# Optimization experiments

Measured on AMD Instinct MI355X. Metric: run time of the kernel, lower is better.

Reference implementation:

```python
import jax, jax.numpy as jnp
import numpy as np

WS = 7           # window side
N = WS * WS      # tokens per window = 49
DIM = 384
H = 12
HD = DIM // H    # 32
BW = 2048        # num_windows * batch
NW = 4           # windows per image (mask batch)
SCALE = 1.0 / float(np.sqrt(HD))


def _rel_index():
    coords = np.stack(np.meshgrid(np.arange(WS), np.arange(WS), indexing='ij'))  # (2,7,7)
    flat = coords.reshape(2, -1)                      # (2,49)
    rel = flat[:, :, None] - flat[:, None, :]         # (2,49,49)
    rel = rel.transpose(1, 2, 0).copy()               # (49,49,2)
    rel[..., 0] += WS - 1
    rel[..., 1] += WS - 1
    rel[..., 0] *= 2 * WS - 1
    return jnp.asarray(rel.sum(-1), dtype=jnp.int32)  # (49,49)


def setup_inputs() -> dict:
    key = jax.random.key(0)
    ks = jax.random.split(key, 16)
    f32 = jnp.float32
    se = jax.random.normal(ks[0], (BW, N, DIM), dtype=f32)
    de = jax.random.normal(ks[1], (BW, N, DIM), dtype=f32)
    mask = jnp.where(jax.random.uniform(ks[2], (NW, N, N)) < 0.1, f32(-1e9), f32(0.0))
    s = 0.02
    w_v_se = jax.random.normal(ks[3], (DIM, DIM), dtype=f32) * s
    b_v_se = jnp.zeros((DIM,), dtype=f32)
    w_qkv = jax.random.normal(ks[4], (3 * DIM, DIM), dtype=f32) * s
    b_qkv = jnp.zeros((3 * DIM,), dtype=f32)
    w_proj_se = jax.random.normal(ks[5], (DIM, DIM), dtype=f32) * s
    b_proj_se = jnp.zeros((DIM,), dtype=f32)
    w_proj_de = jax.random.normal(ks[6], (DIM, DIM), dtype=f32) * s
    b_proj_de = jnp.zeros((DIM,), dtype=f32)
    rpb = jax.random.normal(ks[7], ((2 * WS - 1) ** 2, H), dtype=f32) * s  # (169,12)
    rel_idx = _rel_index()
    return {
        'se': se, 'de': de, 'mask': mask,
        'w_v_se': w_v_se, 'b_v_se': b_v_se,
        'w_qkv': w_qkv, 'b_qkv': b_qkv,
        'w_proj_se': w_proj_se, 'b_proj_se': b_proj_se,
        'w_proj_de': w_proj_de, 'b_proj_de': b_proj_de,
        'rpb': rpb, 'rel_idx': rel_idx,
    }


def reference(se, de, mask, w_v_se, b_v_se, w_qkv, b_qkv,
              w_proj_se, b_proj_se, w_proj_de, b_proj_de, rpb, rel_idx):
    B_, N_, C = se.shape
    # qkv from de (coa=False branch)
    qkv = (de @ w_qkv.T + b_qkv).reshape(B_, N_, 3, H, HD).transpose(2, 0, 3, 1, 4)
    q, k, v_de = qkv[0], qkv[1], qkv[2]                 # (B_,H,N,HD)
    v_se = (se @ w_v_se.T + b_v_se).reshape(B_, N_, H, HD).transpose(0, 2, 1, 3)
    attn = jnp.einsum('bhnd,bhmd->bhnm', q * SCALE, k)  # (B_,H,N,N)
    bias = rpb[rel_idx].transpose(2, 0, 1)              # (H,N,N)
    attn = attn + bias[None]
    # add window mask: view as (B, nW, H, N, N)
    attn = attn.reshape(B_ // NW, NW, H, N_, N_) + mask[None, :, None]
    attn = jax.nn.softmax(attn.reshape(B_, H, N_, N_), axis=-1)
    se_o = jnp.einsum('bhnm,bhmd->bnhd', attn, v_se).reshape(B_, N_, C)
    de_o = jnp.einsum('bhnm,bhmd->bnhd', attn, v_de).reshape(B_, N_, C)
    se_o = se_o @ w_proj_se.T + b_proj_se
    de_o = de_o @ w_proj_de.T + b_proj_de
    return (se_o, de_o)
```

## Files before the change

### kernel.cpp

```cpp
#include <hip/hip_runtime.h>

typedef _Float16 f16;
typedef __attribute__((ext_vector_type(8))) _Float16 f16x8;
typedef __attribute__((ext_vector_type(4))) _Float16 f16x4;
typedef __attribute__((ext_vector_type(4))) float f32x4;

#define MFMA16(a, b, c) __builtin_amdgcn_mfma_f32_16x16x32_f16(a, b, c, 0, 0, 0)

#define SCALE_F 0.17677669529663687f
#define NHEAD 12
#define NTOK 49
#define NBW 2048
#define VTJ 56

#define SCHEDB() __builtin_amdgcn_sched_barrier(0)
#define WAITL0() asm volatile("s_waitcnt lgkmcnt(0)" ::: "memory")

__global__ void cast_weights(const float* __restrict__ wqkv, const float* __restrict__ wvse,
                             const float* __restrict__ wpse, const float* __restrict__ wpde,
                             f16* o_qkv, f16* o_vse, f16* o_pse, f16* o_pde) {
    int i = blockIdx.x * 256 + threadIdx.x;
    if (i >= 221184) return;
    const float* src;
    f16* dst;
    int off;
    if (i < 110592) { src = wqkv; dst = o_qkv; off = i; }
    else if (i < 147456) { src = wvse; dst = o_vse; off = i - 110592; }
    else if (i < 184320) { src = wpse; dst = o_pse; off = i - 147456; }
    else { src = wpde; dst = o_pde; off = i - 184320; }
    f32x4 v = ((const f32x4*)src)[off];
    f16x4 o;
#pragma unroll
    for (int e = 0; e < 4; ++e) o[e] = (f16)v[e];
    ((f16x4*)dst)[off] = o;
}

__global__ void prep_bm(const float* __restrict__ rpb, const int* __restrict__ rel_idx,
                        const float* __restrict__ mask, float* __restrict__ bm) {
    int blk = blockIdx.x;
    int w4 = blk / NHEAD, h = blk - w4 * NHEAD;
    for (int idx = threadIdx.x; idx < 4096; idx += 64) {
        int r = idx >> 6, c = idx & 63;
        float v = -1e30f;
        if (r < NTOK && c < NTOK)
            v = rpb[rel_idx[r * NTOK + c] * NHEAD + h] + mask[(w4 * NTOK + r) * NTOK + c];
        bm[(size_t)blk * 4096 + idx] = v;
    }
}

template <int EPI, bool A_F32, typename OUT_T>
__global__ __launch_bounds__(256) void gemm_bt(const void* __restrict__ Av, const f16* __restrict__ B,
                                               const float* __restrict__ bias, OUT_T* __restrict__ C,
                                               f16* __restrict__ VT, int ldc) {
    __shared__ __align__(16) f16 As[128 * 64];
    __shared__ __align__(16) f16 Bs[128 * 64];
    const int nwg = gridDim.x * gridDim.y;
    int wg = blockIdx.y * gridDim.x + blockIdx.x;
    wg = (wg & 7) * (nwg >> 3) + (wg >> 3);
    const int m0 = (wg / gridDim.x) * 128, n0 = (wg % gridDim.x) * 128;
    const int tid = threadIdx.x;
    const int w = tid >> 6, l = tid & 63;
    const int wm = w >> 1, wn = w & 1;
    const int lr = l & 15, lg = l >> 4;
    const int sp = l & 7;
    const int lrow = l >> 3;

    f32x4 acc[4][4] = {};

    for (int t = 0; t < 6; ++t) {
        __syncthreads();
        if constexpr (A_F32) {
            const float* A32 = (const float*)Av;
            f32x4 t0[4], t1[4];
#pragma unroll
            for (int it = 0; it < 4; ++it) {
                int row = w * 32 + it * 8 + lrow;
                const float* g = A32 + (size_t)(m0 + row) * 384 + t * 64 + sp * 8;
                t0[it] = *(const f32x4*)g;
                t1[it] = *(const f32x4*)(g + 4);
            }
#pragma unroll
            for (int it = 0; it < 4; ++it) {
                int row = w * 32 + it * 8 + lrow;
                f16x8 hx;
#pragma unroll
                for (int e = 0; e < 4; ++e) { hx[e] = (f16)t0[it][e]; hx[e + 4] = (f16)t1[it][e]; }
                *(f16x8*)(As + row * 64 + (sp ^ (row & 7)) * 8) = hx;
            }
#pragma unroll
            for (int it = 0; it < 4; ++it) {
                int row = w * 32 + it * 8 + lrow;
                int gchunk = sp ^ (row & 7);
                const f16* gB = B + (size_t)(n0 + row) * 384 + t * 64 + gchunk * 8;
                f16* lB = Bs + (w * 32 + it * 8) * 64;
                __builtin_amdgcn_global_load_lds((const __attribute__((address_space(1))) void*)gB,
                                                 (__attribute__((address_space(3))) void*)lB, 16, 0, 0);
            }
        } else {
            const f16* A16 = (const f16*)Av;
#pragma unroll
            for (int it = 0; it < 4; ++it) {
                int row = w * 32 + it * 8 + lrow;
                int gchunk = sp ^ (row & 7);
                const f16* gA = A16 + (size_t)(m0 + row) * 384 + t * 64 + gchunk * 8;
                const f16* gB = B + (size_t)(n0 + row) * 384 + t * 64 + gchunk * 8;
                f16* lA = As + (w * 32 + it * 8) * 64;
                f16* lB = Bs + (w * 32 + it * 8) * 64;
                __builtin_amdgcn_global_load_lds((const __attribute__((address_space(1))) void*)gA,
                                                 (__attribute__((address_space(3))) void*)lA, 16, 0, 0);
                __builtin_amdgcn_global_load_lds((const __attribute__((address_space(1))) void*)gB,
                                                 (__attribute__((address_space(3))) void*)lB, 16, 0, 0);
            }
        }
        __syncthreads();
#pragma unroll
        for (int ks = 0; ks < 2; ++ks) {
            f16x8 af[4], bfr[4];
#pragma unroll
            for (int mi = 0; mi < 4; ++mi) {
                int r = 64 * wm + 16 * mi + lr;
                int chunk = (lg + 4 * ks) ^ (r & 7);
                af[mi] = *(const f16x8*)(As + r * 64 + chunk * 8);
            }
#pragma unroll
            for (int ni = 0; ni < 4; ++ni) {
                int r = 64 * wn + 16 * ni + lr;
                int chunk = (lg + 4 * ks) ^ (r & 7);
                bfr[ni] = *(const f16x8*)(Bs + r * 64 + chunk * 8);
            }
            __builtin_amdgcn_s_setprio(1);
#pragma unroll
            for (int mi = 0; mi < 4; ++mi)
#pragma unroll
                for (int ni = 0; ni < 4; ++ni)
                    acc[mi][ni] = MFMA16(af[mi], bfr[ni], acc[mi][ni]);
            __builtin_amdgcn_s_setprio(0);
        }
    }

#pragma unroll
    for (int mi = 0; mi < 4; ++mi) {
#pragma unroll
        for (int ni = 0; ni < 4; ++ni) {
            int col = n0 + 64 * wn + 16 * ni + lr;
            float bv = bias[col];
#pragma unroll
            for (int reg = 0; reg < 4; ++reg) {
                int row = m0 + 64 * wm + 16 * mi + 4 * lg + reg;
                float v = acc[mi][ni][reg] + bv;
                if constexpr (EPI == 0) {
                    C[(size_t)row * ldc + col] = (OUT_T)v;
                } else if constexpr (EPI == 1) {
                    if (col < 384) v *= SCALE_F;
                    C[(size_t)row * ldc + col] = (OUT_T)v;
                } else {
                    int b = row / 49, j = row - b * 49;
                    VT[((size_t)b * NHEAD + (col >> 5)) * (32 * VTJ) + (col & 31) * VTJ + j] = (f16)v;
                }
            }
        }
    }
}

__global__ __launch_bounds__(128) void attn_kernel(const f16* __restrict__ qk,
                                                   const f16* __restrict__ vse_t,
                                                   const f16* __restrict__ vde_t,
                                                   const float* __restrict__ bm_all,
                                                   f16* __restrict__ att_se, f16* __restrict__ att_de) {
    __shared__ __align__(16) f16 Ps[2][64 * 64];

    const int wv = threadIdx.x >> 6;
    const int l = threadIdx.x & 63;
    const int bh = blockIdx.x * 2 + wv;
    const int b = bh / NHEAD, h = bh - b * NHEAD;
    const int lr = l & 15, lg = l >> 4;
    const size_t wbase = (size_t)b * NTOK;
    f16* P = Ps[wv];

    f16x8 qa[4], kb[4];
#pragma unroll
    for (int mi = 0; mi < 4; ++mi)
        qa[mi] = *(const f16x8*)(qk + (wbase + 16 * mi + lr) * 768 + h * 32 + lg * 8);
#pragma unroll
    for (int ni = 0; ni < 4; ++ni)
        kb[ni] = *(const f16x8*)(qk + (wbase + 16 * ni + lr) * 768 + 384 + h * 32 + lg * 8);

    const f32x4 zero4 = {0.f, 0.f, 0.f, 0.f};
    f32x4 S[4][4];
    __builtin_amdgcn_s_setprio(1);
#pragma unroll
    for (int mi = 0; mi < 4; ++mi)
#pragma unroll
        for (int ni = 0; ni < 4; ++ni)
            S[mi][ni] = MFMA16(qa[mi], kb[ni], zero4);
    __builtin_amdgcn_s_setprio(0);

    f16x8 vbr[2][2][2];
#pragma unroll
    for (int s = 0; s < 2; ++s) {
        const f16* vt = (s ? vde_t : vse_t) + (size_t)bh * (32 * VTJ);
#pragma unroll
        for (int ks = 0; ks < 2; ++ks)
#pragma unroll
            for (int ni = 0; ni < 2; ++ni) {
                int j0 = 8 * lg + 32 * ks;
                if (j0 == 56) j0 = 48;
                vbr[s][ks][ni] = *(const f16x8*)(vt + (16 * ni + lr) * VTJ + j0);
            }
    }

    const float* bmp = bm_all + (size_t)((b & 3) * NHEAD + h) * 4096;
#pragma unroll
    for (int mi = 0; mi < 4; ++mi) {
#pragma unroll
        for (int reg = 0; reg < 4; ++reg) {
            int r = 16 * mi + 4 * lg + reg;
            float v[4];
#pragma unroll
            for (int ni = 0; ni < 4; ++ni)
                v[ni] = S[mi][ni][reg] + bmp[(r << 6) + 16 * ni + lr];
            float mx = fmaxf(fmaxf(v[0], v[1]), fmaxf(v[2], v[3]));
#pragma unroll
            for (int off = 1; off < 16; off <<= 1) mx = fmaxf(mx, __shfl_xor(mx, off));
            float e[4];
            float sm = 0.f;
#pragma unroll
            for (int ni = 0; ni < 4; ++ni) {
                e[ni] = __expf(v[ni] - mx);
                sm += e[ni];
            }
#pragma unroll
            for (int off = 1; off < 16; off <<= 1) sm += __shfl_xor(sm, off);
            float inv = 1.f / sm;
#pragma unroll
            for (int ni = 0; ni < 4; ++ni)
                P[(r << 6) + ((16 * ni + lr) ^ ((r & 7) << 3))] = (f16)(e[ni] * inv);
        }
    }
    WAITL0();
    SCHEDB();

#pragma unroll
    for (int s = 0; s < 2; ++s) {
        f32x4 o[4][2] = {};
#pragma unroll
        for (int ks = 0; ks < 2; ++ks) {
            f16x8 pa[4];
#pragma unroll
            for (int mi = 0; mi < 4; ++mi) {
                int r = 16 * mi + lr;
                pa[mi] = *(const f16x8*)(P + (r << 6) + ((8 * lg + 32 * ks) ^ ((r & 7) << 3)));
            }
            __builtin_amdgcn_s_setprio(1);
#pragma unroll
            for (int ni = 0; ni < 2; ++ni)
#pragma unroll
                for (int mi = 0; mi < 4; ++mi) o[mi][ni] = MFMA16(pa[mi], vbr[s][ks][ni], o[mi][ni]);
            __builtin_amdgcn_s_setprio(0);
        }
        f16* dst = s ? att_de : att_se;
#pragma unroll
        for (int mi = 0; mi < 4; ++mi) {
#pragma unroll
            for (int reg = 0; reg < 4; ++reg) {
                int r = 16 * mi + 4 * lg + reg;
                if (r < NTOK) {
#pragma unroll
                    for (int ni = 0; ni < 2; ++ni)
                        dst[(wbase + r) * 384 + h * 32 + 16 * ni + lr] = (f16)o[mi][ni][reg];
                }
            }
        }
    }
}

extern "C" void kernel_launch(void* const* d_in, const int* in_sizes, int n_in,
                              void* d_out, int out_size, void* d_ws, size_t ws_size,
                              hipStream_t stream) {
    const float* se = (const float*)d_in[0];
    const float* de = (const float*)d_in[1];
    const float* mask = (const float*)d_in[2];
    const float* w_v_se = (const float*)d_in[3];
    const float* b_v_se = (const float*)d_in[4];
    const float* w_qkv = (const float*)d_in[5];
    const float* b_qkv = (const float*)d_in[6];
    const float* w_proj_se = (const float*)d_in[7];
    const float* b_proj_se = (const float*)d_in[8];
    const float* w_proj_de = (const float*)d_in[9];
    const float* b_proj_de = (const float*)d_in[10];
    const float* rpb = (const float*)d_in[11];
    const int* rel_idx = (const int*)d_in[12];

    const size_t SE_ELEMS = (size_t)NBW * NTOK * 384;

    char* ws = (char*)d_ws;
    f16* att_se = (f16*)(ws);
    f16* att_de = (f16*)(ws + 77070336);
    f16* qk_h   = (f16*)(ws + 154140672);
    f16* vse_t  = (f16*)(ws + 308281344);
    f16* vde_t  = (f16*)(ws + 396361728);
    f16* wqkv_h = (f16*)(ws + 484442112);
    f16* wvse_h = (f16*)(ws + 485326848);
    f16* wpse_h = (f16*)(ws + 485621760);
    f16* wpde_h = (f16*)(ws + 485916672);
    float* bm   = (float*)(ws + 486211584);

    cast_weights<<<864, 256, 0, stream>>>(w_qkv, w_v_se, w_proj_se, w_proj_de,
                                          wqkv_h, wvse_h, wpse_h, wpde_h);
    prep_bm<<<48, 64, 0, stream>>>(rpb, rel_idx, mask, bm);

    gemm_bt<1, true, f16><<<dim3(6, 784), 256, 0, stream>>>((const void*)de, wqkv_h, b_qkv,
                                                            qk_h, nullptr, 768);
    gemm_bt<2, true, f16><<<dim3(3, 784), 256, 0, stream>>>((const void*)de, wqkv_h + 768 * 384,
                                                            b_qkv + 768, (f16*)nullptr, vde_t, 0);
    gemm_bt<2, true, f16><<<dim3(3, 784), 256, 0, stream>>>((const void*)se, wvse_h, b_v_se,
                                                            (f16*)nullptr, vse_t, 0);

    attn_kernel<<<NBW * NHEAD / 2, 128, 0, stream>>>(qk_h, vse_t, vde_t, bm, att_se, att_de);

    gemm_bt<0, false, float><<<dim3(3, 784), 256, 0, stream>>>((const void*)att_se, wpse_h, b_proj_se,
                                                               (float*)d_out, nullptr, 384);
    gemm_bt<0, false, float><<<dim3(3, 784), 256, 0, stream>>>((const void*)att_de, wpde_h, b_proj_de,
                                                               (float*)d_out + SE_ELEMS, nullptr, 384);
}
```

Before: 726.8 us.

## Use 256x64 GEMM tiles, fuse QKV projection, read V row-major in attention

Replaces the 128x128 GEMM with a 512-thread 256x64 tile kernel. The three input projections become two launches by producing a single fused QKV buffer. The transposed-V scatter epilogue is removed: attention now gathers V directly from the row-major QKV/VSE buffers with strided scalar loads, and applies the softmax scale in attention instead of in the GEMM. This cuts the uncoalesced transposed stores and one launch, at the cost of strided element-wise V loads and less B-tile reuse per block.

```diff
diff --git a/kernel.cpp b/kernel.cpp
--- a/kernel.cpp
+++ b/kernel.cpp
@@ -11,7 +11,6 @@
 #define NHEAD 12
 #define NTOK 49
 #define NBW 2048
-#define VTJ 56
 
 #define SCHEDB() __builtin_amdgcn_sched_barrier(0)
 #define WAITL0() asm volatile("s_waitcnt lgkmcnt(0)" ::: "memory")
@@ -48,89 +47,81 @@
     }
 }
 
-template <int EPI, bool A_F32, typename OUT_T>
-__global__ __launch_bounds__(256) void gemm_bt(const void* __restrict__ Av, const f16* __restrict__ B,
-                                               const float* __restrict__ bias, OUT_T* __restrict__ C,
-                                               f16* __restrict__ VT, int ldc) {
-    __shared__ __align__(16) f16 As[128 * 64];
-    __shared__ __align__(16) f16 Bs[128 * 64];
+template <bool A_F32, typename OUT_T>
+__global__ __launch_bounds__(512, 4) void gemm256(const void* __restrict__ Av, const f16* __restrict__ B,
+                                                  const float* __restrict__ bias, OUT_T* __restrict__ C,
+                                                  int ldc) {
+    __shared__ __align__(16) f16 As[256 * 64];
+    __shared__ __align__(16) f16 Bs[64 * 64];
     const int nwg = gridDim.x * gridDim.y;
     int wg = blockIdx.y * gridDim.x + blockIdx.x;
     wg = (wg & 7) * (nwg >> 3) + (wg >> 3);
-    const int m0 = (wg / gridDim.x) * 128, n0 = (wg % gridDim.x) * 128;
+    const int m0 = (wg / gridDim.x) * 256, n0 = (wg % gridDim.x) * 64;
     const int tid = threadIdx.x;
     const int w = tid >> 6, l = tid & 63;
-    const int wm = w >> 1, wn = w & 1;
     const int lr = l & 15, lg = l >> 4;
-    const int sp = l & 7;
-    const int lrow = l >> 3;
-
-    f32x4 acc[4][4] = {};
+    const int sp = tid & 7;
+    const int lrow = tid >> 3;
+
+    f32x4 acc[2][4] = {};
 
     for (int t = 0; t < 6; ++t) {
         __syncthreads();
         if constexpr (A_F32) {
             const float* A32 = (const float*)Av;
-            f32x4 t0[4], t1[4];
 #pragma unroll
             for (int it = 0; it < 4; ++it) {
-                int row = w * 32 + it * 8 + lrow;
-                const float* g = A32 + (size_t)(m0 + row) * 384 + t * 64 + sp * 8;
-                t0[it] = *(const f32x4*)g;
-                t1[it] = *(const f32x4*)(g + 4);
-            }
-#pragma unroll
-            for (int it = 0; it < 4; ++it) {
-                int row = w * 32 + it * 8 + lrow;
+                int row = it * 64 + lrow;
+                int c = sp ^ (row & 7);
+                const float* g = A32 + (size_t)(m0 + row) * 384 + t * 64 + c * 8;
+                f32x4 t0 = *(const f32x4*)g;
+                f32x4 t1 = *(const f32x4*)(g + 4);
                 f16x8 hx;
 #pragma unroll
-                for (int e = 0; e < 4; ++e) { hx[e] = (f16)t0[it][e]; hx[e + 4] = (f16)t1[it][e]; }
-                *(f16x8*)(As + row * 64 + (sp ^ (row & 7)) * 8) = hx;
-            }
-#pragma unroll
-            for (int it = 0; it < 4; ++it) {
-                int row = w * 32 + it * 8 + lrow;
-                int gchunk = sp ^ (row & 7);
-                const f16* gB = B + (size_t)(n0 + row) * 384 + t * 64 + gchunk * 8;
-                f16* lB = Bs + (w * 32 + it * 8) * 64;
-                __builtin_amdgcn_global_load_lds((const __attribute__((address_space(1))) void*)gB,
-                                                 (__attribute__((address_space(3))) void*)lB, 16, 0, 0);
+                for (int e = 0; e < 4; ++e) { hx[e] = (f16)t0[e]; hx[e + 4] = (f16)t1[e]; }
+                *(f16x8*)(As + row * 64 + sp * 8) = hx;
             }
         } else {
             const f16* A16 = (const f16*)Av;
 #pragma unroll
             for (int it = 0; it < 4; ++it) {
-                int row = w * 32 + it * 8 + lrow;
-                int gchunk = sp ^ (row & 7);
-                const f16* gA = A16 + (size_t)(m0 + row) * 384 + t * 64 + gchunk * 8;
-                const f16* gB = B + (size_t)(n0 + row) * 384 + t * 64 + gchunk * 8;
-                f16* lA = As + (w * 32 + it * 8) * 64;
-                f16* lB = Bs + (w * 32 + it * 8) * 64;
+                int row0 = it * 64 + w * 8;
+                int row = row0 + (l >> 3);
+                int c = (l & 7) ^ (row & 7);
+                const f16* gA = A16 + (size_t)(m0 + row) * 384 + t * 64 + c * 8;
+                f16* lA = As + row0 * 64;
                 __builtin_amdgcn_global_load_lds((const __attribute__((address_space(1))) void*)gA,
                                                  (__attribute__((address_space(3))) void*)lA, 16, 0, 0);
-                __builtin_amdgcn_global_load_lds((const __attribute__((address_space(1))) void*)gB,
-                                                 (__attribute__((address_space(3))) void*)lB, 16, 0, 0);
-            }
+            }
+        }
+        {
+            int row0 = w * 8;
+            int row = row0 + (l >> 3);
+            int c = (l & 7) ^ (row & 7);
+            const f16* gB = B + (size_t)(n0 + row) * 384 + t * 64 + c * 8;
+            f16* lB = Bs + row0 * 64;
+            __builtin_amdgcn_global_load_lds((const __attribute__((address_space(1))) void*)gB,
+                                             (__attribute__((address_space(3))) void*)lB, 16, 0, 0);
         }
         __syncthreads();
 #pragma unroll
         for (int ks = 0; ks < 2; ++ks) {
-            f16x8 af[4], bfr[4];
-#pragma unroll
-            for (int mi = 0; mi < 4; ++mi) {
-                int r = 64 * wm + 16 * mi + lr;
-                int chunk = (lg + 4 * ks) ^ (r & 7);
-                af[mi] = *(const f16x8*)(As + r * 64 + chunk * 8);
+            f16x8 af[2], bfr[4];
+#pragma unroll
+            for (int mi = 0; mi < 2; ++mi) {
+                int r = w * 32 + mi * 16 + lr;
+                int c = (ks * 4 + lg) ^ (r & 7);
+                af[mi] = *(const f16x8*)(As + r * 64 + c * 8);
             }
 #pragma unroll
             for (int ni = 0; ni < 4; ++ni) {
-                int r = 64 * wn + 16 * ni + lr;
-                int chunk = (lg + 4 * ks) ^ (r & 7);
-                bfr[ni] = *(const f16x8*)(Bs + r * 64 + chunk * 8);
+                int r = ni * 16 + lr;
+                int c = (ks * 4 + lg) ^ (r & 7);
+                bfr[ni] = *(const f16x8*)(Bs + r * 64 + c * 8);
             }
             __builtin_amdgcn_s_setprio(1);
 #pragma unroll
-            for (int mi = 0; mi < 4; ++mi)
+            for (int mi = 0; mi < 2; ++mi)
 #pragma unroll
                 for (int ni = 0; ni < 4; ++ni)
                     acc[mi][ni] = MFMA16(af[mi], bfr[ni], acc[mi][ni]);
@@ -139,32 +130,22 @@
     }
 
 #pragma unroll
-    for (int mi = 0; mi < 4; ++mi) {
+    for (int mi = 0; mi < 2; ++mi) {
 #pragma unroll
         for (int ni = 0; ni < 4; ++ni) {
-            int col = n0 + 64 * wn + 16 * ni + lr;
+            int col = n0 + ni * 16 + lr;
             float bv = bias[col];
 #pragma unroll
             for (int reg = 0; reg < 4; ++reg) {
-                int row = m0 + 64 * wm + 16 * mi + 4 * lg + reg;
-                float v = acc[mi][ni][reg] + bv;
-                if constexpr (EPI == 0) {
-                    C[(size_t)row * ldc + col] = (OUT_T)v;
-                } else if constexpr (EPI == 1) {
-                    if (col < 384) v *= SCALE_F;
-                    C[(size_t)row * ldc + col] = (OUT_T)v;
-                } else {
-                    int b = row / 49, j = row - b * 49;
-                    VT[((size_t)b * NHEAD + (col >> 5)) * (32 * VTJ) + (col & 31) * VTJ + j] = (f16)v;
-                }
-            }
-        }
-    }
-}
-
-__global__ __launch_bounds__(128) void attn_kernel(const f16* __restrict__ qk,
-                                                   const f16* __restrict__ vse_t,
-                                                   const f16* __restrict__ vde_t,
+                int row = m0 + w * 32 + mi * 16 + 4 * lg + reg;
+                C[(size_t)row * ldc + col] = (OUT_T)(acc[mi][ni][reg] + bv);
+            }
+        }
+    }
+}
+
+__global__ __launch_bounds__(128) void attn_kernel(const f16* __restrict__ qkv,
+                                                   const f16* __restrict__ vse,
                                                    const float* __restrict__ bm_all,
                                                    f16* __restrict__ att_se, f16* __restrict__ att_de) {
     __shared__ __align__(16) f16 Ps[2][64 * 64];
@@ -180,10 +161,10 @@
     f16x8 qa[4], kb[4];
 #pragma unroll
     for (int mi = 0; mi < 4; ++mi)
-        qa[mi] = *(const f16x8*)(qk + (wbase + 16 * mi + lr) * 768 + h * 32 + lg * 8);
+        qa[mi] = *(const f16x8*)(qkv + (wbase + 16 * mi + lr) * 1152 + h * 32 + lg * 8);
 #pragma unroll
     for (int ni = 0; ni < 4; ++ni)
-        kb[ni] = *(const f16x8*)(qk + (wbase + 16 * ni + lr) * 768 + 384 + h * 32 + lg * 8);
+        kb[ni] = *(const f16x8*)(qkv + (wbase + 16 * ni + lr) * 1152 + 384 + h * 32 + lg * 8);
 
     const f32x4 zero4 = {0.f, 0.f, 0.f, 0.f};
     f32x4 S[4][4];
@@ -198,14 +179,15 @@
     f16x8 vbr[2][2][2];
 #pragma unroll
     for (int s = 0; s < 2; ++s) {
-        const f16* vt = (s ? vde_t : vse_t) + (size_t)bh * (32 * VTJ);
+        const f16* vbase = s ? (qkv + wbase * 1152 + 768 + h * 32) : (vse + wbase * 384 + h * 32);
+        const int RS = s ? 1152 : 384;
 #pragma unroll
         for (int ks = 0; ks < 2; ++ks)
 #pragma unroll
             for (int ni = 0; ni < 2; ++ni) {
-                int j0 = 8 * lg + 32 * ks;
-                if (j0 == 56) j0 = 48;
-                vbr[s][ks][ni] = *(const f16x8*)(vt + (16 * ni + lr) * VTJ + j0);
+                const f16* p = vbase + (size_t)(8 * lg + 32 * ks) * RS + 16 * ni + lr;
+#pragma unroll
+                for (int e = 0; e < 8; ++e) vbr[s][ks][ni][e] = p[(size_t)e * RS];
             }
     }
 
@@ -218,7 +200,7 @@
             float v[4];
 #pragma unroll
             for (int ni = 0; ni < 4; ++ni)
-                v[ni] = S[mi][ni][reg] + bmp[(r << 6) + 16 * ni + lr];
+                v[ni] = S[mi][ni][reg] * SCALE_F + bmp[(r << 6) + 16 * ni + lr];
             float mx = fmaxf(fmaxf(v[0], v[1]), fmaxf(v[2], v[3]));
 #pragma unroll
             for (int off = 1; off < 16; off <<= 1) mx = fmaxf(mx, __shfl_xor(mx, off));
@@ -296,30 +278,25 @@
     char* ws = (char*)d_ws;
     f16* att_se = (f16*)(ws);
     f16* att_de = (f16*)(ws + 77070336);
-    f16* qk_h   = (f16*)(ws + 154140672);
-    f16* vse_t  = (f16*)(ws + 308281344);
-    f16* vde_t  = (f16*)(ws + 396361728);
-    f16* wqkv_h = (f16*)(ws + 484442112);
-    f16* wvse_h = (f16*)(ws + 485326848);
-    f16* wpse_h = (f16*)(ws + 485621760);
-    f16* wpde_h = (f16*)(ws + 485916672);
-    float* bm   = (float*)(ws + 486211584);
+    f16* qkv_h  = (f16*)(ws + 154140672);
+    f16* vse_h  = (f16*)(ws + 385351680);
+    f16* wqkv_h = (f16*)(ws + 462422016);
+    f16* wvse_h = (f16*)(ws + 463306752);
+    f16* wpse_h = (f16*)(ws + 463601664);
+    f16* wpde_h = (f16*)(ws + 463896576);
+    float* bm   = (float*)(ws + 464191488);
 
     cast_weights<<<864, 256, 0, stream>>>(w_qkv, w_v_se, w_proj_se, w_proj_de,
                                           wqkv_h, wvse_h, wpse_h, wpde_h);
     prep_bm<<<48, 64, 0, stream>>>(rpb, rel_idx, mask, bm);
 
-    gemm_bt<1, true, f16><<<dim3(6, 784), 256, 0, stream>>>((const void*)de, wqkv_h, b_qkv,
-                                                            qk_h, nullptr, 768);
-    gemm_bt<2, true, f16><<<dim3(3, 784), 256, 0, stream>>>((const void*)de, wqkv_h + 768 * 384,
-                                                            b_qkv + 768, (f16*)nullptr, vde_t, 0);
-    gemm_bt<2, true, f16><<<dim3(3, 784), 256, 0, stream>>>((const void*)se, wvse_h, b_v_se,
-                                                            (f16*)nullptr, vse_t, 0);
-
-    attn_kernel<<<NBW * NHEAD / 2, 128, 0, stream>>>(qk_h, vse_t, vde_t, bm, att_se, att_de);
-
-    gemm_bt<0, false, float><<<dim3(3, 784), 256, 0, stream>>>((const void*)att_se, wpse_h, b_proj_se,
-                                                               (float*)d_out, nullptr, 384);
-    gemm_bt<0, false, float><<<dim3(3, 784), 256, 0, stream>>>((const void*)att_de, wpde_h, b_proj_de,
-                                                               (float*)d_out + SE_ELEMS, nullptr, 384);
-}
+    gemm256<true, f16><<<dim3(18, 392), 512, 0, stream>>>((const void*)de, wqkv_h, b_qkv, qkv_h, 1152);
+    gemm256<true, f16><<<dim3(6, 392), 512, 0, stream>>>((const void*)se, wvse_h, b_v_se, vse_h, 384);
+
+    attn_kernel<<<NBW * NHEAD / 2, 128, 0, stream>>>(qkv_h, vse_h, bm, att_se, att_de);
+
+    gemm256<false, float><<<dim3(6, 392), 512, 0, stream>>>((const void*)att_se, wpse_h, b_proj_se,
+                                                            (float*)d_out, 384);
+    gemm256<false, float><<<dim3(6, 392), 512, 0, stream>>>((const void*)att_de, wpde_h, b_proj_de,
+                                                            (float*)d_out + SE_ELEMS, 384);
+}
```

New measurement: 722.6 us. About the same (-0.6%).
